# Optimization experiments

Measured on AMD Instinct MI355X. Metric: run time of the kernel, lower is better.

Reference implementation:

```python
import jax, jax.numpy as jnp
import numpy as np

NF, NC, LENGTH, BATCH = 64, 16, 2048, 256
WEIGHT_BI, WEIGHT_L2 = 0.01, 0.01
BETA = 2.5     # temporal soft-min/max sharpness (TemporalOperator beta=2.5)
KAPPA = 10.0   # logical soft-min/max sharpness (avm approximation)
EPSN = 1e-12


def setup_inputs() -> dict:
    key = jax.random.key(0)
    ks = jax.random.split(key, 11)
    x = jax.random.normal(ks[0], (BATCH, LENGTH, 2), dtype=jnp.float32)
    t1 = jax.random.uniform(ks[1], (NF,), minval=0.0, maxval=float(LENGTH // 2), dtype=jnp.float32)
    t2 = jax.random.uniform(ks[2], (NF,), minval=float(LENGTH // 2), maxval=float(LENGTH), dtype=jnp.float32)
    a = jax.random.uniform(ks[3], (NF,), dtype=jnp.float32)
    b = jax.random.uniform(ks[4], (NF,), dtype=jnp.float32)
    p1 = jax.random.uniform(ks[5], (NC, NF), dtype=jnp.float32)
    p2 = jax.random.uniform(ks[6], (1, NC), dtype=jnp.float32)
    tvar_temporal = jax.random.uniform(ks[7], (NF,), dtype=jnp.float32)
    tvar_logical1 = jax.random.uniform(ks[8], (NC,), dtype=jnp.float32)
    tvar_logical2 = jax.random.uniform(ks[9], (1,), dtype=jnp.float32)
    eps = jnp.full((1,), 0.1, dtype=jnp.float32)
    return dict(x=x, t1=t1, t2=t2, a=a, b=b, p1=p1, p2=p2,
                tvar_temporal=tvar_temporal, tvar_logical1=tvar_logical1,
                tvar_logical2=tvar_logical2, eps=eps)


def _ste(v, v_new):
    # torch clamps parameter .data under no_grad -> value changes, grad is identity
    return v + jax.lax.stop_gradient(v_new - v)


def _wsel(r, logw, sharp):
    # weighted soft-max (sharp>0) / soft-min (sharp<0) along last axis
    s = jax.nn.softmax(sharp * r + logw, axis=-1)
    return jnp.sum(s * r, axis=-1)


def reference(x, t1, t2, a, b, p1, p2, tvar_temporal, tvar_logical1, tvar_logical2, eps):
    # --- in-place parameter maintenance (clamp under no_grad in torch) ---
    p1 = _ste(p1, jnp.clip(p1, 0.0, 1.0))
    p2 = _ste(p2, jnp.clip(p2, 0.0, 1.0))
    tvt = _ste(tvar_temporal, jnp.clip(tvar_temporal, 0.0, 1.0))
    tvl1 = _ste(tvar_logical1, jnp.clip(tvar_logical1, 0.0, 1.0))
    tvl2 = _ste(tvar_logical2, jnp.clip(tvar_logical2, 0.0, 1.0))
    t1c = jnp.clip(t1, 0.0, LENGTH - 1.0)
    t2c = jnp.clip(t2, 0.0, LENGTH - 1.0)
    t1c = jnp.where(t1c >= t2c - 1.0, t2c - 1.0, t1c)
    t1u = _ste(t1, t1c)
    t2u = _ste(t2, t2c)

    # --- predicates (vectorized over all nf features; dim = i % 2) ---
    dims = jnp.arange(NF) % 2
    rp = a[None, None, :] * x[:, :, dims] - b[None, None, :]     # [B, T, NF]
    rp = jnp.transpose(rp, (0, 2, 1))                             # [B, NF, T]

    # --- temporal operators: smooth window [t1, t2] + soft min/max over time ---
    tg = jnp.arange(LENGTH, dtype=x.dtype)
    w = jax.nn.sigmoid(BETA * (tg[None, :] - t1u[:, None])) * \
        jax.nn.sigmoid(BETA * (t2u[:, None] - tg[None, :]))       # [NF, T]
    logw = jnp.log(w + EPSN)[None]                                # [1, NF, T]
    rmax = _wsel(rp, logw, BETA)                                  # eventually  [B, NF]
    rmin = _wsel(rp, logw, -BETA)                                 # always      [B, NF]
    r1 = tvt[None, :] * rmax + (1.0 - tvt[None, :]) * rmin        # [B, NF]

    # --- logical layer 1: weighted soft OR/AND over features, per clause ---
    logp1 = jnp.log(p1 + EPSN)[None]                              # [1, NC, NF]
    r1e = r1[:, None, :]                                          # [B, NC, NF]
    r_or = _wsel(r1e, logp1, KAPPA)
    r_and = _wsel(r1e, logp1, -KAPPA)
    r2 = tvl1[None, :] * r_or + (1.0 - tvl1[None, :]) * r_and     # [B, NC]

    # --- logical layer 2: combine clauses ---
    logp2 = jnp.log(p2[0] + EPSN)[None]                           # [1, NC]
    r_or2 = _wsel(r2, logp2, KAPPA)
    r_and2 = _wsel(r2, logp2, -KAPPA)
    r = tvl2[0] * r_or2 + (1.0 - tvl2[0]) * r_and2                # [B]

    # --- regularizers ---
    bi = WEIGHT_BI * (jnp.sum(tvt * (1.0 - tvt)) + jnp.sum(tvl1 * (1.0 - tvl1)) +
                      jnp.sum(tvl2 * (1.0 - tvl2)) + jnp.sum(p1 * (1.0 - p1)) +
                      jnp.sum(p2 * (1.0 - p2)))
    l2 = WEIGHT_L2 * (jnp.sum(p1 * p1) + jnp.sum(p2 * p2))
    reg = bi + l2
    return r, reg
```

## Files before the change

kernel.cpp:

```cpp
#include <hip/hip_runtime.h>
#include <math.h>

#define NF 64
#define NC 16
#define LEN 2048
#define BATCH 256
#define BETA 2.5f
#define KAPPA 10.0f
#define EPSN 1e-12f
#define LOG2E 1.4426950408889634f

#define TPB 1024
#define NQ (TPB / NF)
#define CHUNK (LEN / NQ)

__device__ __forceinline__ float clip01(float v) { return fminf(fmaxf(v, 0.0f), 1.0f); }

__device__ __forceinline__ float fexp2(float x) {
#if __has_builtin(__builtin_amdgcn_exp2f)
    return __builtin_amdgcn_exp2f(x);
#else
    return exp2f(x);
#endif
}

__device__ __forceinline__ float frcp(float x) {
#if __has_builtin(__builtin_amdgcn_rcpf)
    return __builtin_amdgcn_rcpf(x);
#else
    return 1.0f / x;
#endif
}

#define LW_BLOCKS ((NF * LEN / 4) / 256)

__global__ __launch_bounds__(256) void lw_reg_kernel(
    const float* __restrict__ t1, const float* __restrict__ t2,
    const float* __restrict__ p1, const float* __restrict__ p2,
    const float* __restrict__ tvt, const float* __restrict__ tvl1,
    const float* __restrict__ tvl2, float4* __restrict__ lwT4,
    float* __restrict__ out) {
    const int bid = blockIdx.x;
    const int tid = threadIdx.x;

    if (bid == LW_BLOCKS) {
        __shared__ float red[256];
        float acc = 0.0f;
        for (int i = tid; i < NC * NF; i += 256) {
            float p = clip01(p1[i]);
            acc += 0.01f * (p * (1.0f - p)) + 0.01f * (p * p);
        }
        if (tid < NC) {
            float p = clip01(p2[tid]);
            acc += 0.01f * (p * (1.0f - p)) + 0.01f * (p * p);
        }
        if (tid < NF) {
            float c = clip01(tvt[tid]);
            acc += 0.01f * (c * (1.0f - c));
        }
        if (tid < NC) {
            float c = clip01(tvl1[tid]);
            acc += 0.01f * (c * (1.0f - c));
        }
        if (tid == 0) {
            float c = clip01(tvl2[0]);
            acc += 0.01f * (c * (1.0f - c));
        }
        red[tid] = acc;
        __syncthreads();
        for (int s = 128; s > 0; s >>= 1) {
            if (tid < s) red[tid] += red[tid + s];
            __syncthreads();
        }
        if (tid == 0) out[BATCH] = red[0];
        return;
    }

    int idx = bid * 256 + tid;
    int f = idx & (NF - 1);
    int g = idx >> 6;
    float t1c = fminf(fmaxf(t1[f], 0.0f), (float)(LEN - 1));
    float t2c = fminf(fmaxf(t2[f], 0.0f), (float)(LEN - 1));
    t1c = fminf(t1c, t2c - 1.0f);
    float4 r;
#pragma unroll
    for (int j = 0; j < 4; ++j) {
        float t = (float)(4 * g + j);
        float su = 1.0f / (1.0f + __expf(-BETA * (t - t1c)));
        float sv = 1.0f / (1.0f + __expf(-BETA * (t2c - t)));
        ((float*)&r)[j] = __log2f(su * sv + EPSN);
    }
    lwT4[idx] = r;
}

__global__ __launch_bounds__(TPB) void fused_main(
    const float* __restrict__ x, const float4* __restrict__ lwT4,
    const float* __restrict__ av, const float* __restrict__ bv,
    const float* __restrict__ p1, const float* __restrict__ p2,
    const float* __restrict__ tvt_, const float* __restrict__ tvl1_,
    const float* __restrict__ tvl2_, float* __restrict__ out) {
    __shared__ float4 redQ[NQ][NF];
    __shared__ float r1s[NF];
    __shared__ float r2s[NC];

    const int b = blockIdx.x;
    const int tid = threadIdx.x;
    const int f = tid & (NF - 1);
    const int q = tid >> 6;
    const int ch = f & 1;

    const float B2 = BETA * LOG2E;
    const float KL = KAPPA * LOG2E;
    const float A2 = B2 * av[f];

    const int t0 = q * CHUNK;
    const float4* lw4 = lwT4 + (t0 >> 2) * NF + f;
    const float4* xp4 = (const float4*)(x + (size_t)b * (LEN * 2) + 2 * t0);

    float Sp0 = 0.f, Xp0 = 0.f, Sm0 = 0.f, Xm0 = 0.f;
    float Sp1 = 0.f, Xp1 = 0.f, Sm1 = 0.f, Xm1 = 0.f;
#pragma unroll 4
    for (int g = 0; g < CHUNK / 4; ++g) {
        float4 lw = lw4[g * NF];
        float4 u0 = xp4[2 * g];
        float4 u1 = xp4[2 * g + 1];
        float xa = ch ? u0.y : u0.x;
        float xb = ch ? u0.w : u0.z;
        float xc = ch ? u1.y : u1.x;
        float xd = ch ? u1.w : u1.z;
        float e;
        e = fexp2(fmaf(A2, xa, lw.x));  Sp0 += e; Xp0 = fmaf(e, xa, Xp0);
        e = fexp2(fmaf(-A2, xa, lw.x)); Sm0 += e; Xm0 = fmaf(e, xa, Xm0);
        e = fexp2(fmaf(A2, xb, lw.y));  Sp1 += e; Xp1 = fmaf(e, xb, Xp1);
        e = fexp2(fmaf(-A2, xb, lw.y)); Sm1 += e; Xm1 = fmaf(e, xb, Xm1);
        e = fexp2(fmaf(A2, xc, lw.z));  Sp0 += e; Xp0 = fmaf(e, xc, Xp0);
        e = fexp2(fmaf(-A2, xc, lw.z)); Sm0 += e; Xm0 = fmaf(e, xc, Xm0);
        e = fexp2(fmaf(A2, xd, lw.w));  Sp1 += e; Xp1 = fmaf(e, xd, Xp1);
        e = fexp2(fmaf(-A2, xd, lw.w)); Sm1 += e; Xm1 = fmaf(e, xd, Xm1);
    }

    redQ[q][f] = make_float4(Sp0 + Sp1, Xp0 + Xp1, Sm0 + Sm1, Xm0 + Xm1);
    __syncthreads();
    if (tid >= 64) return;

    const int l = tid;
    float ax = 0.f, ay = 0.f, az = 0.f, aw = 0.f;
#pragma unroll
    for (int s = 0; s < NQ; ++s) {
        float4 v = redQ[s][l];
        ax += v.x; ay += v.y; az += v.z; aw += v.w;
    }
    {
        float af = av[l], bf = bv[l];
        float tvt = clip01(tvt_[l]);
        float rmax = af * (ay / ax);
        float rmin = af * (aw / az);
        r1s[l] = tvt * rmax + (1.0f - tvt) * rmin - bf;
    }

    {
        const int c = l & 15;
        const int j = l >> 4;
        float so = 0.f, wo = 0.f, sa = 0.f, wa = 0.f;
#pragma unroll
        for (int i = 0; i < 16; ++i) {
            int ff = j * 16 + i;
            float r1v = r1s[ff];
            float lg = __log2f(clip01(p1[c * NF + ff]) + EPSN);
            float z = KL * r1v;
            float eo = fexp2(z + lg);
            float ea = fexp2(lg - z);
            so += eo; wo = fmaf(eo, r1v, wo);
            sa += ea; wa = fmaf(ea, r1v, wa);
        }
#pragma unroll
        for (int d = 16; d < 64; d <<= 1) {
            so += __shfl_xor(so, d);
            wo += __shfl_xor(wo, d);
            sa += __shfl_xor(sa, d);
            wa += __shfl_xor(wa, d);
        }
        if (l < NC) {
            float tvl1 = clip01(tvl1_[l]);
            r2s[l] = tvl1 * (wo / so) + (1.0f - tvl1) * (wa / sa);
        }
    }

    if (l == 0) {
        float so = 0.f, wo = 0.f, sa = 0.f, wa = 0.f;
#pragma unroll
        for (int c = 0; c < NC; ++c) {
            float lg = __log2f(clip01(p2[c]) + EPSN);
            float r2v = r2s[c];
            float z = KL * r2v;
            float eo = fexp2(z + lg);
            float ea = fexp2(lg - z);
            so += eo; wo = fmaf(eo, r2v, wo);
            sa += ea; wa = fmaf(ea, r2v, wa);
        }
        float tvl2 = clip01(tvl2_[0]);
        out[b] = tvl2 * (wo / so) + (1.0f - tvl2) * (wa / sa);
    }
}

__global__ __launch_bounds__(TPB) void fused_inline(
    const float* __restrict__ x, const float* __restrict__ t1g,
    const float* __restrict__ t2g, const float* __restrict__ av,
    const float* __restrict__ bv, const float* __restrict__ p1,
    const float* __restrict__ p2, const float* __restrict__ tvt_,
    const float* __restrict__ tvl1_, const float* __restrict__ tvl2_,
    float* __restrict__ out) {
    __shared__ float4 redQ[NQ][NF];
    __shared__ float r1s[NF];
    __shared__ float r2s[NC];

    const int b = blockIdx.x;
    const int tid = threadIdx.x;
    const int f = tid & (NF - 1);
    const int q = tid >> 6;
    const int ch = f & 1;

    const float B2 = BETA * LOG2E;
    const float KL = KAPPA * LOG2E;
    const float A2 = B2 * av[f];

    float t1c = fminf(fmaxf(t1g[f], 0.0f), (float)(LEN - 1));
    float t2c = fminf(fmaxf(t2g[f], 0.0f), (float)(LEN - 1));
    t1c = fminf(t1c, t2c - 1.0f);
    const float c1 = B2 * t1c;
    const float c2 = -B2 * t2c;

    const int t0 = q * CHUNK;
    const float4* xp4 = (const float4*)(x + (size_t)b * (LEN * 2) + 2 * t0);

    float Sp0 = 0.f, Xp0 = 0.f, Sm0 = 0.f, Xm0 = 0.f;
    float Sp1 = 0.f, Xp1 = 0.f, Sm1 = 0.f, Xm1 = 0.f;
#pragma unroll 4
    for (int k2 = 0; k2 < CHUNK / 2; ++k2) {
        float4 v = xp4[k2];
        float xa = ch ? v.y : v.x;
        float xb = ch ? v.w : v.z;
        float tfa = (float)(t0 + 2 * k2);
        float tfb = tfa + 1.0f;
        {
            float g1 = fmaf(-B2, tfa, c1);
            float g2 = fmaf(B2, tfa, c2);
            float den = (1.0f + fexp2(g1)) * (1.0f + fexp2(g2));
            float w = frcp(den);
            float P = fexp2(A2 * xa);
            float Pm = frcp(P);
            float tp = P * w, tm = Pm * w;
            Sp0 += tp; Xp0 = fmaf(tp, xa, Xp0);
            Sm0 += tm; Xm0 = fmaf(tm, xa, Xm0);
        }
        {
            float g1 = fmaf(-B2, tfb, c1);
            float g2 = fmaf(B2, tfb, c2);
            float den = (1.0f + fexp2(g1)) * (1.0f + fexp2(g2));
            float w = frcp(den);
            float P = fexp2(A2 * xb);
            float Pm = frcp(P);
            float tp = P * w, tm = Pm * w;
            Sp1 += tp; Xp1 = fmaf(tp, xb, Xp1);
            Sm1 += tm; Xm1 = fmaf(tm, xb, Xm1);
        }
    }

    redQ[q][f] = make_float4(Sp0 + Sp1, Xp0 + Xp1, Sm0 + Sm1, Xm0 + Xm1);

    if (b == 0 && q == NQ - 1) {
        const int l = f;
        float acc = 0.0f;
#pragma unroll
        for (int i = 0; i < 16; ++i) {
            float p = clip01(p1[i * NF + l]);
            acc += 0.01f * (p * (1.0f - p)) + 0.01f * (p * p);
        }
        {
            float c = clip01(tvt_[l]);
            acc += 0.01f * (c * (1.0f - c));
        }
        if (l < NC) {
            float p = clip01(p2[l]);
            acc += 0.01f * (p * (1.0f - p)) + 0.01f * (p * p);
            float c = clip01(tvl1_[l]);
            acc += 0.01f * (c * (1.0f - c));
        }
        if (l == 0) {
            float c = clip01(tvl2_[0]);
            acc += 0.01f * (c * (1.0f - c));
        }
#pragma unroll
        for (int d = 1; d < 64; d <<= 1) acc += __shfl_xor(acc, d);
        if (l == 0) out[BATCH] = acc;
    }

    __syncthreads();
    if (tid >= 64) return;

    const int l = tid;
    float ax = 0.f, ay = 0.f, az = 0.f, aw = 0.f;
#pragma unroll
    for (int s = 0; s < NQ; ++s) {
        float4 v = redQ[s][l];
        ax += v.x; ay += v.y; az += v.z; aw += v.w;
    }
    {
        float af = av[l], bf = bv[l];
        float tvt = clip01(tvt_[l]);
        float rmax = af * (ay / ax);
        float rmin = af * (aw / az);
        r1s[l] = tvt * rmax + (1.0f - tvt) * rmin - bf;
    }
    {
        const int c = l & 15;
        const int j = l >> 4;
        float so = 0.f, wo = 0.f, sa = 0.f, wa = 0.f;
#pragma unroll
        for (int i = 0; i < 16; ++i) {
            int ff = j * 16 + i;
            float r1v = r1s[ff];
            float lg = __log2f(clip01(p1[c * NF + ff]) + EPSN);
            float z = KL * r1v;
            float eo = fexp2(z + lg);
            float ea = fexp2(lg - z);
            so += eo; wo = fmaf(eo, r1v, wo);
            sa += ea; wa = fmaf(ea, r1v, wa);
        }
#pragma unroll
        for (int d = 16; d < 64; d <<= 1) {
            so += __shfl_xor(so, d);
            wo += __shfl_xor(wo, d);
            sa += __shfl_xor(sa, d);
            wa += __shfl_xor(wa, d);
        }
        if (l < NC) {
            float tvl1 = clip01(tvl1_[l]);
            r2s[l] = tvl1 * (wo / so) + (1.0f - tvl1) * (wa / sa);
        }
    }
    if (l == 0) {
        float so = 0.f, wo = 0.f, sa = 0.f, wa = 0.f;
#pragma unroll
        for (int c = 0; c < NC; ++c) {
            float lg = __log2f(clip01(p2[c]) + EPSN);
            float r2v = r2s[c];
            float z = KL * r2v;
            float eo = fexp2(z + lg);
            float ea = fexp2(lg - z);
            so += eo; wo = fmaf(eo, r2v, wo);
            sa += ea; wa = fmaf(ea, r2v, wa);
        }
        float tvl2 = clip01(tvl2_[0]);
        out[b] = tvl2 * (wo / so) + (1.0f - tvl2) * (wa / sa);
    }
}

extern "C" void kernel_launch(void* const* d_in, const int* in_sizes, int n_in,
                              void* d_out, int out_size, void* d_ws, size_t ws_size,
                              hipStream_t stream) {
    const float* x    = (const float*)d_in[0];
    const float* t1   = (const float*)d_in[1];
    const float* t2   = (const float*)d_in[2];
    const float* a    = (const float*)d_in[3];
    const float* bv   = (const float*)d_in[4];
    const float* p1   = (const float*)d_in[5];
    const float* p2   = (const float*)d_in[6];
    const float* tvt  = (const float*)d_in[7];
    const float* tvl1 = (const float*)d_in[8];
    const float* tvl2 = (const float*)d_in[9];
    float* out = (float*)d_out;

    const size_t lw_bytes = (size_t)(NF * LEN) * sizeof(float);

    if (d_ws && ws_size >= lw_bytes) {
        float4* lwT4 = (float4*)d_ws;
        lw_reg_kernel<<<LW_BLOCKS + 1, 256, 0, stream>>>(t1, t2, p1, p2, tvt, tvl1,
                                                         tvl2, lwT4, out);
        fused_main<<<BATCH, TPB, 0, stream>>>(x, lwT4, a, bv, p1, p2,
                                              tvt, tvl1, tvl2, out);
    } else {
        fused_inline<<<BATCH, TPB, 0, stream>>>(x, t1, t2, a, bv, p1, p2,
                                                tvt, tvl1, tvl2, out);
    }
}
```

Measured before the change: 26.05 us.

## Restrict temporal softmax to each feature's window with dynamic per-wave feature scheduling

Stores the log-window table feature-major and restructures fused_main so each wavefront grabs one feature at a time through a shared atomic counter. It sums only over time steps between roughly t1-16 and t2+18, where the sigmoid window weight is not negligible, and reduces with wave shuffles instead of a shared-memory cross-quarter reduction. This skips exp work on time steps whose weights are effectively zero and balances uneven window lengths across waves. It also moves the regularizer computation into block 0. In exchange, each thread now reads x with a strided pattern per feature, so x is re-read once per feature from cache, and dropping the tails is an approximation.

```diff
diff --git a/kernel.cpp b/kernel.cpp
--- a/kernel.cpp
+++ b/kernel.cpp
@@ -11,8 +11,9 @@
 #define LOG2E 1.4426950408889634f
 
 #define TPB 1024
-#define NQ (TPB / NF)
-#define CHUNK (LEN / NQ)
+
+#define FBQ (TPB / NF)
+#define FBCHUNK (LEN / FBQ)
 
 __device__ __forceinline__ float clip01(float v) { return fminf(fmaxf(v, 0.0f), 1.0f); }
 
@@ -38,7 +39,7 @@
     const float* __restrict__ t1, const float* __restrict__ t2,
     const float* __restrict__ p1, const float* __restrict__ p2,
     const float* __restrict__ tvt, const float* __restrict__ tvl1,
-    const float* __restrict__ tvl2, float4* __restrict__ lwT4,
+    const float* __restrict__ tvl2, float4* __restrict__ lwF4,
     float* __restrict__ out) {
     const int bid = blockIdx.x;
     const int tid = threadIdx.x;
@@ -77,8 +78,8 @@
     }
 
     int idx = bid * 256 + tid;
-    int f = idx & (NF - 1);
-    int g = idx >> 6;
+    int f = idx >> 9;
+    int g = idx & 511;
     float t1c = fminf(fmaxf(t1[f], 0.0f), (float)(LEN - 1));
     float t2c = fminf(fmaxf(t2[f], 0.0f), (float)(LEN - 1));
     t1c = fminf(t1c, t2c - 1.0f);
@@ -90,73 +91,113 @@
         float sv = 1.0f / (1.0f + __expf(-BETA * (t2c - t)));
         ((float*)&r)[j] = __log2f(su * sv + EPSN);
     }
-    lwT4[idx] = r;
+    lwF4[idx] = r;
 }
 
 __global__ __launch_bounds__(TPB) void fused_main(
-    const float* __restrict__ x, const float4* __restrict__ lwT4,
+    const float* __restrict__ x, const float4* __restrict__ lwF4,
+    const float* __restrict__ t1g, const float* __restrict__ t2g,
     const float* __restrict__ av, const float* __restrict__ bv,
     const float* __restrict__ p1, const float* __restrict__ p2,
     const float* __restrict__ tvt_, const float* __restrict__ tvl1_,
     const float* __restrict__ tvl2_, float* __restrict__ out) {
-    __shared__ float4 redQ[NQ][NF];
+    __shared__ int fcnt;
     __shared__ float r1s[NF];
     __shared__ float r2s[NC];
 
     const int b = blockIdx.x;
     const int tid = threadIdx.x;
-    const int f = tid & (NF - 1);
-    const int q = tid >> 6;
-    const int ch = f & 1;
+    const int l = tid & 63;
 
     const float B2 = BETA * LOG2E;
     const float KL = KAPPA * LOG2E;
-    const float A2 = B2 * av[f];
-
-    const int t0 = q * CHUNK;
-    const float4* lw4 = lwT4 + (t0 >> 2) * NF + f;
-    const float4* xp4 = (const float4*)(x + (size_t)b * (LEN * 2) + 2 * t0);
-
-    float Sp0 = 0.f, Xp0 = 0.f, Sm0 = 0.f, Xm0 = 0.f;
-    float Sp1 = 0.f, Xp1 = 0.f, Sm1 = 0.f, Xm1 = 0.f;
-#pragma unroll 4
-    for (int g = 0; g < CHUNK / 4; ++g) {
-        float4 lw = lw4[g * NF];
-        float4 u0 = xp4[2 * g];
-        float4 u1 = xp4[2 * g + 1];
-        float xa = ch ? u0.y : u0.x;
-        float xb = ch ? u0.w : u0.z;
-        float xc = ch ? u1.y : u1.x;
-        float xd = ch ? u1.w : u1.z;
-        float e;
-        e = fexp2(fmaf(A2, xa, lw.x));  Sp0 += e; Xp0 = fmaf(e, xa, Xp0);
-        e = fexp2(fmaf(-A2, xa, lw.x)); Sm0 += e; Xm0 = fmaf(e, xa, Xm0);
-        e = fexp2(fmaf(A2, xb, lw.y));  Sp1 += e; Xp1 = fmaf(e, xb, Xp1);
-        e = fexp2(fmaf(-A2, xb, lw.y)); Sm1 += e; Xm1 = fmaf(e, xb, Xm1);
-        e = fexp2(fmaf(A2, xc, lw.z));  Sp0 += e; Xp0 = fmaf(e, xc, Xp0);
-        e = fexp2(fmaf(-A2, xc, lw.z)); Sm0 += e; Xm0 = fmaf(e, xc, Xm0);
-        e = fexp2(fmaf(A2, xd, lw.w));  Sp1 += e; Xp1 = fmaf(e, xd, Xp1);
-        e = fexp2(fmaf(-A2, xd, lw.w)); Sm1 += e; Xm1 = fmaf(e, xd, Xm1);
-    }
-
-    redQ[q][f] = make_float4(Sp0 + Sp1, Xp0 + Xp1, Sm0 + Sm1, Xm0 + Xm1);
+
+    if (tid == 0) fcnt = 0;
     __syncthreads();
+
+    const float4* xb4 = (const float4*)(x + (size_t)b * (LEN * 2));
+
+    for (;;) {
+        int f;
+        if (l == 0) f = atomicAdd(&fcnt, 1);
+        f = __shfl(f, 0);
+        if (f >= NF) break;
+
+        float t1c = fminf(fmaxf(t1g[f], 0.0f), (float)(LEN - 1));
+        float t2c = fminf(fmaxf(t2g[f], 0.0f), (float)(LEN - 1));
+        t1c = fminf(t1c, t2c - 1.0f);
+        int lo = (int)t1c - 16; lo = (lo < 0 ? 0 : lo) & ~3;
+        int hi = (int)t2c + 18; hi = (hi > LEN ? LEN : hi);
+
+        const float A2 = B2 * av[f];
+        const int ch = f & 1;
+        const float4* lwf = lwF4 + f * (LEN / 4);
+
+        float Sp = 0.f, Xp = 0.f, Sm = 0.f, Xm = 0.f;
+        for (int T = lo; T < hi; T += 256) {
+            int t = T + 4 * l;
+            if (t < LEN) {
+                float4 lw = lwf[t >> 2];
+                float4 u0 = xb4[t >> 1];
+                float4 u1 = xb4[(t >> 1) + 1];
+                float xa = ch ? u0.y : u0.x;
+                float xb_ = ch ? u0.w : u0.z;
+                float xc = ch ? u1.y : u1.x;
+                float xd = ch ? u1.w : u1.z;
+                float e;
+                e = fexp2(fmaf(A2, xa, lw.x));   Sp += e; Xp = fmaf(e, xa, Xp);
+                e = fexp2(fmaf(-A2, xa, lw.x));  Sm += e; Xm = fmaf(e, xa, Xm);
+                e = fexp2(fmaf(A2, xb_, lw.y));  Sp += e; Xp = fmaf(e, xb_, Xp);
+                e = fexp2(fmaf(-A2, xb_, lw.y)); Sm += e; Xm = fmaf(e, xb_, Xm);
+                e = fexp2(fmaf(A2, xc, lw.z));   Sp += e; Xp = fmaf(e, xc, Xp);
+                e = fexp2(fmaf(-A2, xc, lw.z));  Sm += e; Xm = fmaf(e, xc, Xm);
+                e = fexp2(fmaf(A2, xd, lw.w));   Sp += e; Xp = fmaf(e, xd, Xp);
+                e = fexp2(fmaf(-A2, xd, lw.w));  Sm += e; Xm = fmaf(e, xd, Xm);
+            }
+        }
+#pragma unroll
+        for (int d = 1; d < 64; d <<= 1) {
+            Sp += __shfl_xor(Sp, d);
+            Xp += __shfl_xor(Xp, d);
+            Sm += __shfl_xor(Sm, d);
+            Xm += __shfl_xor(Xm, d);
+        }
+        if (l == 0) {
+            float af = av[f], bf = bv[f];
+            float tvt = clip01(tvt_[f]);
+            r1s[f] = tvt * (af * (Xp / Sp)) + (1.0f - tvt) * (af * (Xm / Sm)) - bf;
+        }
+    }
+
+    __syncthreads();
+
+    if (b == 0 && tid >= 64 && tid < 128) {
+        float acc = 0.0f;
+#pragma unroll
+        for (int i = 0; i < 16; ++i) {
+            float p = clip01(p1[i * NF + l]);
+            acc += 0.01f * (p * (1.0f - p)) + 0.01f * (p * p);
+        }
+        {
+            float c = clip01(tvt_[l]);
+            acc += 0.01f * (c * (1.0f - c));
+        }
+        if (l < NC) {
+            float p = clip01(p2[l]);
+            acc += 0.01f * (p * (1.0f - p)) + 0.01f * (p * p);
+            float c = clip01(tvl1_[l]);
+            acc += 0.01f * (c * (1.0f - c));
+        }
+        if (l == 0) {
+            float c = clip01(tvl2_[0]);
+            acc += 0.01f * (c * (1.0f - c));
+        }
+#pragma unroll
+        for (int d = 1; d < 64; d <<= 1) acc += __shfl_xor(acc, d);
+        if (l == 0) out[BATCH] = acc;
+    }
+
     if (tid >= 64) return;
-
-    const int l = tid;
-    float ax = 0.f, ay = 0.f, az = 0.f, aw = 0.f;
-#pragma unroll
-    for (int s = 0; s < NQ; ++s) {
-        float4 v = redQ[s][l];
-        ax += v.x; ay += v.y; az += v.z; aw += v.w;
-    }
-    {
-        float af = av[l], bf = bv[l];
-        float tvt = clip01(tvt_[l]);
-        float rmax = af * (ay / ax);
-        float rmin = af * (aw / az);
-        r1s[l] = tvt * rmax + (1.0f - tvt) * rmin - bf;
-    }
 
     {
         const int c = l & 15;
@@ -210,7 +251,7 @@
     const float* __restrict__ p2, const float* __restrict__ tvt_,
     const float* __restrict__ tvl1_, const float* __restrict__ tvl2_,
     float* __restrict__ out) {
-    __shared__ float4 redQ[NQ][NF];
+    __shared__ float4 redQ[FBQ][NF];
     __shared__ float r1s[NF];
     __shared__ float r2s[NC];
 
@@ -230,13 +271,12 @@
     const float c1 = B2 * t1c;
     const float c2 = -B2 * t2c;
 
-    const int t0 = q * CHUNK;
+    const int t0 = q * FBCHUNK;
     const float4* xp4 = (const float4*)(x + (size_t)b * (LEN * 2) + 2 * t0);
 
-    float Sp0 = 0.f, Xp0 = 0.f, Sm0 = 0.f, Xm0 = 0.f;
-    float Sp1 = 0.f, Xp1 = 0.f, Sm1 = 0.f, Xm1 = 0.f;
+    float Sp = 0.f, Xp = 0.f, Sm = 0.f, Xm = 0.f;
 #pragma unroll 4
-    for (int k2 = 0; k2 < CHUNK / 2; ++k2) {
+    for (int k2 = 0; k2 < FBCHUNK / 2; ++k2) {
         float4 v = xp4[k2];
         float xa = ch ? v.y : v.x;
         float xb = ch ? v.w : v.z;
@@ -250,8 +290,8 @@
             float P = fexp2(A2 * xa);
             float Pm = frcp(P);
             float tp = P * w, tm = Pm * w;
-            Sp0 += tp; Xp0 = fmaf(tp, xa, Xp0);
-            Sm0 += tm; Xm0 = fmaf(tm, xa, Xm0);
+            Sp += tp; Xp = fmaf(tp, xa, Xp);
+            Sm += tm; Xm = fmaf(tm, xa, Xm);
         }
         {
             float g1 = fmaf(-B2, tfb, c1);
@@ -261,14 +301,14 @@
             float P = fexp2(A2 * xb);
             float Pm = frcp(P);
             float tp = P * w, tm = Pm * w;
-            Sp1 += tp; Xp1 = fmaf(tp, xb, Xp1);
-            Sm1 += tm; Xm1 = fmaf(tm, xb, Xm1);
-        }
-    }
-
-    redQ[q][f] = make_float4(Sp0 + Sp1, Xp0 + Xp1, Sm0 + Sm1, Xm0 + Xm1);
-
-    if (b == 0 && q == NQ - 1) {
+            Sp += tp; Xp = fmaf(tp, xb, Xp);
+            Sm += tm; Xm = fmaf(tm, xb, Xm);
+        }
+    }
+
+    redQ[q][f] = make_float4(Sp, Xp, Sm, Xm);
+
+    if (b == 0 && q == FBQ - 1) {
         const int l = f;
         float acc = 0.0f;
 #pragma unroll
@@ -301,7 +341,7 @@
     const int l = tid;
     float ax = 0.f, ay = 0.f, az = 0.f, aw = 0.f;
 #pragma unroll
-    for (int s = 0; s < NQ; ++s) {
+    for (int s = 0; s < FBQ; ++s) {
         float4 v = redQ[s][l];
         ax += v.x; ay += v.y; az += v.z; aw += v.w;
     }
@@ -374,10 +414,10 @@
     const size_t lw_bytes = (size_t)(NF * LEN) * sizeof(float);
 
     if (d_ws && ws_size >= lw_bytes) {
-        float4* lwT4 = (float4*)d_ws;
+        float4* lwF4 = (float4*)d_ws;
         lw_reg_kernel<<<LW_BLOCKS + 1, 256, 0, stream>>>(t1, t2, p1, p2, tvt, tvl1,
-                                                         tvl2, lwT4, out);
-        fused_main<<<BATCH, TPB, 0, stream>>>(x, lwT4, a, bv, p1, p2,
+                                                         tvl2, lwF4, out);
+        fused_main<<<BATCH, TPB, 0, stream>>>(x, lwF4, t1, t2, a, bv, p1, p2,
                                               tvt, tvl1, tvl2, out);
     } else {
         fused_inline<<<BATCH, TPB, 0, stream>>>(x, t1, t2, a, bv, p1, p2,
```

Result: slower. 26.65 us (+2.3%).
